# Kernel optimization log

Hardware: AMD Instinct MI355X
Metric: run time of the kernel (lower is better)

Reference implementation:

```python
import jax, jax.numpy as jnp
import numpy as np

EPS = 1e-5  # torch BatchNorm1d default eps

# BinActive: sign forward, straight-through estimator backward (grad clipped where |x|>1)
@jax.custom_vjp
def bin_active(x):
    return jnp.sign(x)

def _ba_fwd(x):
    return jnp.sign(x), x

def _ba_bwd(x, g):
    return (g * (jnp.abs(x) <= 1.0).astype(g.dtype),)

bin_active.defvjp(_ba_fwd, _ba_bwd)

# XNOR-style weight binarization: sign(W) * mean(|W|) per output column, STE backward
@jax.custom_vjp
def bin_weight(w):
    alpha = jnp.mean(jnp.abs(w), axis=0, keepdims=True)  # [1, out]
    return jnp.sign(w) * alpha

def _bw_fwd(w):
    alpha = jnp.mean(jnp.abs(w), axis=0, keepdims=True)
    return jnp.sign(w) * alpha, w

def _bw_bwd(w, g):
    return (g * (jnp.abs(w) <= 1.0).astype(g.dtype),)

bin_weight.defvjp(_bw_fwd, _bw_bwd)


def setup_inputs() -> dict:
    key = jax.random.key(0)
    ks = jax.random.split(key, 8)
    N, E, IN, H, OUT = 100000, 1600000, 256, 128, 40
    x = jax.random.normal(ks[0], (N, IN), dtype=jnp.float32)
    edge_index = jax.random.randint(ks[1], (2, E), 0, N, dtype=jnp.int64)
    W0 = jax.random.normal(ks[2], (IN, H), dtype=jnp.float32) * (2.0 / IN) ** 0.5
    b0 = jnp.zeros((H,), dtype=jnp.float32)
    W1 = jax.random.normal(ks[3], (H, H), dtype=jnp.float32) * (2.0 / H) ** 0.5
    b1 = jnp.zeros((H,), dtype=jnp.float32)
    W2 = jax.random.normal(ks[4], (H, OUT), dtype=jnp.float32) * (2.0 / H) ** 0.5
    b2 = jnp.zeros((OUT,), dtype=jnp.float32)
    return {"x": x, "edge_index": edge_index, "W0": W0, "b0": b0,
            "W1": W1, "b1": b1, "W2": W2, "b2": b2}


def reference(x, edge_index, W0, b0, W1, b1, W2, b2):
    n = x.shape[0]
    loop = jnp.arange(n, dtype=edge_index.dtype)
    src = jnp.concatenate([edge_index[0], loop])  # add self loops (GCN norm)
    dst = jnp.concatenate([edge_index[1], loop])
    deg = jax.ops.segment_sum(jnp.ones_like(src, dtype=x.dtype), dst, num_segments=n)
    dinv = jnp.where(deg > 0, deg ** -0.5, 0.0)
    norm = (dinv[src] * dinv[dst])[:, None]  # [E+N, 1]

    # BatchNorm1d(affine=False), training-mode batch statistics (biased var)
    mu = jnp.mean(x, axis=0)
    var = jnp.var(x, axis=0)
    h = (x - mu) * jax.lax.rsqrt(var + EPS)

    for W, b in ((W0, b0), (W1, b1), (W2, b2)):
        h = bin_active(h)                       # sign binarize (dropout skipped: eval)
        h = h @ bin_weight(W)                   # binary-weight linear
        h = jax.ops.segment_sum(h[src] * norm, dst, num_segments=n) + b  # D^-1/2 (A+I) D^-1/2 agg
    return jax.nn.log_softmax(h, axis=1)
```

## Files before the change

kernel.cpp:

```cpp
#include <hip/hip_runtime.h>
#include <math.h>

#define IN_DIM 256
#define HD 128
#define OUT_DIM 40
#define S2_STRIDE 64
#define NB_CS 1024
#define NXCD 8

__device__ __forceinline__ int xcc_id() {
    int x;
    asm volatile("s_getreg_b32 %0, hwreg(HW_REG_XCC_ID)" : "=s"(x));
    return x & (NXCD - 1);
}

__global__ __launch_bounds__(256) void k_init(unsigned* deg8b, float* muacc8, int NW8) {
    int i = blockIdx.x * 256 + threadIdx.x;
    if (i < NW8) deg8b[i] = 0u;
    if (i < NXCD * 256) muacc8[i] = 0.f;
}

__global__ __launch_bounds__(256) void k_fuse1(const float* __restrict__ x, int N,
                                               float* __restrict__ muacc8,
                                               const int* __restrict__ ei, int E,
                                               unsigned* __restrict__ deg8b, int NW,
                                               int* __restrict__ rank, int ebl,
                                               const float* __restrict__ W0,
                                               const float* __restrict__ W1,
                                               const float* __restrict__ W2,
                                               unsigned long long* W0p,
                                               unsigned long long* W1p,
                                               unsigned long long* W2p,
                                               float* aS0, float* aS1, float* aS2) {
    __shared__ float lds[256];
    int b = blockIdx.x, tid = threadIdx.x;
    if (b < NB_CS) {
        size_t F4 = (size_t)N * (IN_DIM / 4);
        size_t stride = (size_t)NB_CS * 256;
        float a0 = 0.f, a1 = 0.f, a2 = 0.f, a3 = 0.f;
        const float4* x4 = (const float4*)x;
        for (size_t i = (size_t)b * 256 + tid; i < F4; i += stride) {
            float4 v = x4[i];
            a0 += v.x; a1 += v.y; a2 += v.z; a3 += v.w;
        }
        lds[tid] = 0.f;
        __syncthreads();
        int c0 = (tid * 4) & 255;
        atomicAdd(&lds[c0], a0);
        atomicAdd(&lds[c0 + 1], a1);
        atomicAdd(&lds[c0 + 2], a2);
        atomicAdd(&lds[c0 + 3], a3);
        __syncthreads();
        int xc = xcc_id();
        __hip_atomic_fetch_add(&muacc8[xc * 256 + tid], lds[tid],
                               __ATOMIC_RELAXED, __HIP_MEMORY_SCOPE_WORKGROUP);
    } else if (b < NB_CS + ebl) {
        int e = (b - NB_CS) * 256 + tid;
        if (e < E) {
            int d = ei[E + e];
            int xc = xcc_id();
            int sh = 8 * (d & 3);
            unsigned old = __hip_atomic_fetch_add(&deg8b[(size_t)xc * NW + (d >> 2)],
                                                  1u << sh,
                                                  __ATOMIC_RELAXED, __HIP_MEMORY_SCOPE_WORKGROUP);
            rank[e] = (int)((old >> sh) & 0xFFu) | (xc << 28);
        }
    } else {
        int b2 = b - NB_CS - ebl;
        int lane = tid & 63, w = tid >> 6;
        if (b2 < 32) {
            int j = b2 * 4 + w;
            float asum = 0.f;
            unsigned long long words[4];
            #pragma unroll
            for (int q = 0; q < 4; ++q) {
                float v = W0[(size_t)(4 * lane + q) * HD + j];
                asum += fabsf(v);
                words[q] = __ballot(v < 0.f);
            }
            #pragma unroll
            for (int off = 32; off; off >>= 1) asum += __shfl_xor(asum, off);
            if (lane == 0) {
                aS0[j] = 2.f * asum / 256.f;
                #pragma unroll
                for (int q = 0; q < 4; ++q) W0p[j * 4 + q] = words[q];
            }
        } else if (b2 < 64) {
            int j = (b2 - 32) * 4 + w;
            int fl = lane & 15, kk = lane >> 4;
            float asum = 0.f;
            unsigned long long words[2];
            #pragma unroll
            for (int q = 0; q < 2; ++q) {
                float v = W1[(size_t)(fl * 8 + 4 * q + kk) * HD + j];
                asum += fabsf(v);
                words[q] = __ballot(v < 0.f);
            }
            #pragma unroll
            for (int off = 32; off; off >>= 1) asum += __shfl_xor(asum, off);
            if (lane == 0) {
                aS1[j] = 2.f * asum / 128.f;
                W1p[j * 2 + 0] = words[0];
                W1p[j * 2 + 1] = words[1];
            }
        } else {
            int j = (b2 - 64) * 4 + w;
            int fl = lane & 15, kk = lane >> 4;
            if (j < OUT_DIM) {
                float asum = 0.f;
                unsigned long long words[2];
                #pragma unroll
                for (int q = 0; q < 2; ++q) {
                    float v = W2[(size_t)(fl * 8 + 4 * q + kk) * OUT_DIM + j];
                    asum += fabsf(v);
                    words[q] = __ballot(v < 0.f);
                }
                #pragma unroll
                for (int off = 32; off; off >>= 1) asum += __shfl_xor(asum, off);
                if (lane == 0) {
                    aS2[j] = 2.f * asum / 128.f;
                    W2p[j * 2 + 0] = words[0];
                    W2p[j * 2 + 1] = words[1];
                }
            }
        }
    }
}

__global__ __launch_bounds__(256) void k_bp(const unsigned* __restrict__ deg8b, int NW, int N,
                                            int* bp, unsigned long long* __restrict__ xoffp,
                                            float* __restrict__ dinv, int* __restrict__ cnt) {
    __shared__ int sm[256];
    int i = blockIdx.x * 256 + threadIdx.x;
    int c = 0;
    if (i < N) {
        int w = i >> 2, sh = 8 * (i & 3);
        int run = 0;
        unsigned long long pack = 0;
        #pragma unroll
        for (int xc = 0; xc < NXCD; ++xc) {
            unsigned bc = (deg8b[(size_t)xc * NW + w] >> sh) & 0xFFu;
            pack |= (unsigned long long)(unsigned)run << (8 * xc);
            run += (int)bc;
        }
        xoffp[i] = pack;
        c = run;
        cnt[i] = run;
        dinv[i] = (float)(1.0 / sqrt((double)(run + 1)));
    }
    sm[threadIdx.x] = c;
    __syncthreads();
    for (int off = 128; off; off >>= 1) {
        if (threadIdx.x < off) sm[threadIdx.x] += sm[threadIdx.x + off];
        __syncthreads();
    }
    if (threadIdx.x == 0) bp[blockIdx.x] = sm[0];
}

__global__ __launch_bounds__(512) void k_scanbp(const int* __restrict__ bp, int NB, int* bps,
                                                const float* __restrict__ muacc8,
                                                float* __restrict__ mu) {
    __shared__ int sm[512];
    int t = threadIdx.x;
    if (t < 256) {
        float s = 0.f;
        #pragma unroll
        for (int xc = 0; xc < NXCD; ++xc) s += muacc8[xc * 256 + t];
        mu[t] = s;
    }
    int v = (t < NB) ? bp[t] : 0;
    sm[t] = v;
    __syncthreads();
    for (int off = 1; off < 512; off <<= 1) {
        int add = (t >= off) ? sm[t - off] : 0;
        __syncthreads();
        sm[t] += add;
        __syncthreads();
    }
    if (t < NB) bps[t] = sm[t] - v;
}

__global__ __launch_bounds__(256) void k_rowptr(const int* __restrict__ cnt,
                                                const int* __restrict__ bps, int N, int E,
                                                int* row_ptr) {
    __shared__ int wsum[4];
    int t = threadIdx.x, lane = t & 63, w = t >> 6;
    int i = blockIdx.x * 256 + t;
    int c = (i < N) ? cnt[i] : 0;
    int v = c;
    #pragma unroll
    for (int off = 1; off < 64; off <<= 1) {
        int n = __shfl_up(v, off);
        if (lane >= off) v += n;
    }
    if (lane == 63) wsum[w] = v;
    __syncthreads();
    int wo = 0;
    for (int k = 0; k < w; ++k) wo += wsum[k];
    int excl = bps[blockIdx.x] + wo + v - c;
    if (i < N) row_ptr[i] = excl;
    if (blockIdx.x == 0 && t == 0) row_ptr[N] = E;
}

__global__ __launch_bounds__(256) void k_fuse2(const int* __restrict__ ei, int E,
                                               const int* __restrict__ rowp,
                                               const int* __restrict__ rank,
                                               const unsigned long long* __restrict__ xoffp,
                                               int* __restrict__ cs4, int nbScat,
                                               const float* __restrict__ x,
                                               const float* __restrict__ muacc, float inv_n,
                                               const unsigned long long* __restrict__ W0p,
                                               unsigned char* __restrict__ S0, int N) {
    __shared__ unsigned long long w0s[576];
    int b = blockIdx.x, tid = threadIdx.x;
    if (b < nbScat) {
        int e = b * 256 + tid;
        if (e >= E) return;
        int s = ei[e];
        int d = ei[E + e];
        unsigned r = (unsigned)rank[e];
        int xc = (int)(r >> 28);
        int lr = (int)(r & 0xFFu);
        int xo = (int)((xoffp[d] >> (8 * xc)) & 0xFFu);
        int pos = rowp[d] + xo + lr;
        __builtin_nontemporal_store(s, &cs4[pos]);
    } else {
        {
            int i = tid;
            w0s[9 * (i >> 3) + (i & 7)] = W0p[i];
            i = tid + 256;
            w0s[9 * (i >> 3) + (i & 7)] = W0p[i];
        }
        __syncthreads();
        int lane = tid & 63;
        int row = (b - nbScat) * 4 + (tid >> 6);
        if (row >= N) return;
        float4 xv = ((const float4*)(x + (size_t)row * IN_DIM))[lane];
        float4 ms = ((const float4*)muacc)[lane];
        unsigned long long xw[4];
        xw[0] = __ballot(xv.x < ms.x * inv_n);
        xw[1] = __ballot(xv.y < ms.y * inv_n);
        xw[2] = __ballot(xv.z < ms.z * inv_n);
        xw[3] = __ballot(xv.w < ms.w * inv_n);
        unsigned int pack = 0;
        #pragma unroll
        for (int t2 = 0; t2 < 2; ++t2) {
            const unsigned long long* wc = &w0s[9 * lane + 4 * t2];
            int dd = __popcll(xw[0] ^ wc[0]) + __popcll(xw[1] ^ wc[1]) +
                     __popcll(xw[2] ^ wc[2]) + __popcll(xw[3] ^ wc[3]);
            int S = IN_DIM - 2 * dd;
            int s8 = S >> 1;
            if (s8 > 127) s8 = 127;
            pack |= ((unsigned int)(s8 + 128) & 0xffu) << (8 * t2);
        }
        *(unsigned short*)(S0 + (size_t)row * HD + 2 * lane) = (unsigned short)pack;
    }
}

template <int OUTC>
__global__ __launch_bounds__(256) void k_agg_mm(const unsigned char* __restrict__ Sin,
                                                const int* __restrict__ row_ptr,
                                                const int* __restrict__ cs4,
                                                const float* __restrict__ dinv,
                                                const float* __restrict__ alphaS,
                                                const float* __restrict__ bias,
                                                const unsigned long long* __restrict__ Wnp,
                                                unsigned char* __restrict__ Sout, int N) {
    __shared__ unsigned long long wsm[OUTC * 2 + OUTC / 4 + 8];
    int tid = threadIdx.x;
    for (int i = tid; i < OUTC * 2; i += 256) wsm[9 * (i >> 3) + (i & 7)] = Wnp[i];
    __syncthreads();
    int lane = tid & 63;
    int d = blockIdx.x * 4 + (tid >> 6);
    if (d >= N) return;
    int sub = lane >> 4;
    int fl  = lane & 15;
    float dv = dinv[d];
    float acc[8];
    #pragma unroll
    for (int k = 0; k < 8; ++k) acc[k] = 0.f;
    if (sub == 0) {
        float nrm = dv * dv;
        unsigned long long r = *(const unsigned long long*)(Sin + (size_t)d * HD + fl * 8);
        unsigned int lo = (unsigned int)r, hi = (unsigned int)(r >> 32);
        #pragma unroll
        for (int k = 0; k < 4; ++k) {
            acc[k]     = fmaf(nrm, (float)((lo >> (8 * k)) & 0xffu) - 128.f, acc[k]);
            acc[k + 4] = fmaf(nrm, (float)((hi >> (8 * k)) & 0xffu) - 128.f, acc[k + 4]);
        }
    }
    int e0 = row_ptr[d], e1 = row_ptr[d + 1];
    int e = e0 + sub;
    for (; e + 12 < e1; e += 16) {
        int s0_ = cs4[e], s1_ = cs4[e + 4], s2_ = cs4[e + 8], s3_ = cs4[e + 12];
        float n0 = dinv[s0_] * dv, n1 = dinv[s1_] * dv;
        float n2 = dinv[s2_] * dv, n3 = dinv[s3_] * dv;
        unsigned long long r0 = *(const unsigned long long*)(Sin + (size_t)s0_ * HD + fl * 8);
        unsigned long long r1 = *(const unsigned long long*)(Sin + (size_t)s1_ * HD + fl * 8);
        unsigned long long r2 = *(const unsigned long long*)(Sin + (size_t)s2_ * HD + fl * 8);
        unsigned long long r3 = *(const unsigned long long*)(Sin + (size_t)s3_ * HD + fl * 8);
        #pragma unroll
        for (int k = 0; k < 4; ++k) {
            acc[k]     = fmaf(n0, (float)(((unsigned int)r0 >> (8 * k)) & 0xffu) - 128.f, acc[k]);
            acc[k + 4] = fmaf(n0, (float)(((unsigned int)(r0 >> 32) >> (8 * k)) & 0xffu) - 128.f, acc[k + 4]);
            acc[k]     = fmaf(n1, (float)(((unsigned int)r1 >> (8 * k)) & 0xffu) - 128.f, acc[k]);
            acc[k + 4] = fmaf(n1, (float)(((unsigned int)(r1 >> 32) >> (8 * k)) & 0xffu) - 128.f, acc[k + 4]);
            acc[k]     = fmaf(n2, (float)(((unsigned int)r2 >> (8 * k)) & 0xffu) - 128.f, acc[k]);
            acc[k + 4] = fmaf(n2, (float)(((unsigned int)(r2 >> 32) >> (8 * k)) & 0xffu) - 128.f, acc[k + 4]);
            acc[k]     = fmaf(n3, (float)(((unsigned int)r3 >> (8 * k)) & 0xffu) - 128.f, acc[k]);
            acc[k + 4] = fmaf(n3, (float)(((unsigned int)(r3 >> 32) >> (8 * k)) & 0xffu) - 128.f, acc[k + 4]);
        }
    }
    for (; e + 4 < e1; e += 8) {
        int sa = cs4[e], sb = cs4[e + 4];
        float na = dinv[sa] * dv, nb = dinv[sb] * dv;
        unsigned long long ra = *(const unsigned long long*)(Sin + (size_t)sa * HD + fl * 8);
        unsigned long long rb = *(const unsigned long long*)(Sin + (size_t)sb * HD + fl * 8);
        unsigned int la = (unsigned int)ra, ha = (unsigned int)(ra >> 32);
        unsigned int lb = (unsigned int)rb, hb = (unsigned int)(rb >> 32);
        #pragma unroll
        for (int k = 0; k < 4; ++k) {
            acc[k]     = fmaf(na, (float)((la >> (8 * k)) & 0xffu) - 128.f, acc[k]);
            acc[k + 4] = fmaf(na, (float)((ha >> (8 * k)) & 0xffu) - 128.f, acc[k + 4]);
            acc[k]     = fmaf(nb, (float)((lb >> (8 * k)) & 0xffu) - 128.f, acc[k]);
            acc[k + 4] = fmaf(nb, (float)((hb >> (8 * k)) & 0xffu) - 128.f, acc[k + 4]);
        }
    }
    if (e < e1) {
        int s = cs4[e];
        float nrm = dinv[s] * dv;
        unsigned long long r = *(const unsigned long long*)(Sin + (size_t)s * HD + fl * 8);
        unsigned int lo = (unsigned int)r, hi = (unsigned int)(r >> 32);
        #pragma unroll
        for (int k = 0; k < 4; ++k) {
            acc[k]     = fmaf(nrm, (float)((lo >> (8 * k)) & 0xffu) - 128.f, acc[k]);
            acc[k + 4] = fmaf(nrm, (float)((hi >> (8 * k)) & 0xffu) - 128.f, acc[k + 4]);
        }
    }
    #pragma unroll
    for (int k = 0; k < 8; ++k) {
        acc[k] += __shfl_xor(acc[k], 16);
        acc[k] += __shfl_xor(acc[k], 32);
    }
    unsigned int m8 = 0;
    #pragma unroll
    for (int k = 0; k < 8; ++k) {
        int f = fl * 8 + k;
        float v = alphaS[f] * acc[k] + bias[f];
        if (v < 0.f) m8 |= (1u << k);
    }
    unsigned long long x0 = 0, x1 = 0;
    #pragma unroll
    for (int k = 0; k < 4; ++k) {
        unsigned long long bk = __ballot((m8 >> k) & 1u);
        x0 |= (bk & 0xffffULL) << (16 * k);
    }
    #pragma unroll
    for (int k = 4; k < 8; ++k) {
        unsigned long long bk = __ballot((m8 >> k) & 1u);
        x1 |= (bk & 0xffffULL) << (16 * (k - 4));
    }
    if (OUTC == 128) {
        unsigned int pack = 0;
        #pragma unroll
        for (int t2 = 0; t2 < 2; ++t2) {
            int j = 2 * lane + t2;
            int i0 = j * 2;
            const unsigned long long* wc = &wsm[9 * (i0 >> 3) + (i0 & 7)];
            int dd = __popcll(x0 ^ wc[0]) + __popcll(x1 ^ wc[1]);
            int S = HD - 2 * dd;
            pack |= ((unsigned int)((S >> 1) + 128) & 0xffu) << (8 * t2);
        }
        *(unsigned short*)(Sout + (size_t)d * HD + 2 * lane) = (unsigned short)pack;
    } else {
        int p8 = 128;
        if (lane < OUTC) {
            int i0 = lane * 2;
            const unsigned long long* wc = &wsm[9 * (i0 >> 3) + (i0 & 7)];
            int dd = __popcll(x0 ^ wc[0]) + __popcll(x1 ^ wc[1]);
            p8 = ((HD - 2 * dd) >> 1) + 128;
        }
        Sout[(size_t)d * S2_STRIDE + lane] = (unsigned char)p8;
    }
}

__global__ __launch_bounds__(256) void k_agg_out(const unsigned char* __restrict__ S2,
                                                 const int* __restrict__ row_ptr,
                                                 const int* __restrict__ cs4,
                                                 const float* __restrict__ dinv,
                                                 const float* __restrict__ alphaS2,
                                                 const float* __restrict__ b2,
                                                 float* __restrict__ out, int N) {
    int tid = threadIdx.x, lane = tid & 63;
    int d = blockIdx.x * 4 + (tid >> 6);
    if (d >= N) return;
    int sub = lane >> 4;
    int fl  = lane & 15;
    float dv = dinv[d];
    float acc[4] = {0.f, 0.f, 0.f, 0.f};
    if (sub == 0) {
        float nrm = dv * dv;
        unsigned int r4 = *(const unsigned int*)(S2 + (size_t)d * S2_STRIDE + fl * 4);
        #pragma unroll
        for (int k = 0; k < 4; ++k)
            acc[k] = fmaf(nrm, (float)((r4 >> (8 * k)) & 0xffu) - 128.f, acc[k]);
    }
    int e0 = row_ptr[d], e1 = row_ptr[d + 1];
    int e = e0 + sub;
    for (; e + 12 < e1; e += 16) {
        int s0_ = cs4[e], s1_ = cs4[e + 4], s2_ = cs4[e + 8], s3_ = cs4[e + 12];
        float n0 = dinv[s0_] * dv, n1 = dinv[s1_] * dv;
        float n2 = dinv[s2_] * dv, n3 = dinv[s3_] * dv;
        unsigned int r0 = *(const unsigned int*)(S2 + (size_t)s0_ * S2_STRIDE + fl * 4);
        unsigned int r1 = *(const unsigned int*)(S2 + (size_t)s1_ * S2_STRIDE + fl * 4);
        unsigned int r2 = *(const unsigned int*)(S2 + (size_t)s2_ * S2_STRIDE + fl * 4);
        unsigned int r3 = *(const unsigned int*)(S2 + (size_t)s3_ * S2_STRIDE + fl * 4);
        #pragma unroll
        for (int k = 0; k < 4; ++k) {
            acc[k] = fmaf(n0, (float)((r0 >> (8 * k)) & 0xffu) - 128.f, acc[k]);
            acc[k] = fmaf(n1, (float)((r1 >> (8 * k)) & 0xffu) - 128.f, acc[k]);
            acc[k] = fmaf(n2, (float)((r2 >> (8 * k)) & 0xffu) - 128.f, acc[k]);
            acc[k] = fmaf(n3, (float)((r3 >> (8 * k)) & 0xffu) - 128.f, acc[k]);
        }
    }
    for (; e + 4 < e1; e += 8) {
        int sa = cs4[e], sb = cs4[e + 4];
        float na = dinv[sa] * dv, nb = dinv[sb] * dv;
        unsigned int ra = *(const unsigned int*)(S2 + (size_t)sa * S2_STRIDE + fl * 4);
        unsigned int rb = *(const unsigned int*)(S2 + (size_t)sb * S2_STRIDE + fl * 4);
        #pragma unroll
        for (int k = 0; k < 4; ++k) {
            acc[k] = fmaf(na, (float)((ra >> (8 * k)) & 0xffu) - 128.f, acc[k]);
            acc[k] = fmaf(nb, (float)((rb >> (8 * k)) & 0xffu) - 128.f, acc[k]);
        }
    }
    if (e < e1) {
        int s = cs4[e];
        float nrm = dinv[s] * dv;
        unsigned int r4 = *(const unsigned int*)(S2 + (size_t)s * S2_STRIDE + fl * 4);
        #pragma unroll
        for (int k = 0; k < 4; ++k)
            acc[k] = fmaf(nrm, (float)((r4 >> (8 * k)) & 0xffu) - 128.f, acc[k]);
    }
    #pragma unroll
    for (int k = 0; k < 4; ++k) {
        acc[k] += __shfl_xor(acc[k], 16);
        acc[k] += __shfl_xor(acc[k], 32);
    }
    float h[4];
    float mymax = -INFINITY;
    #pragma unroll
    for (int k = 0; k < 4; ++k) {
        int f = fl * 4 + k;
        h[k] = (f < OUT_DIM) ? (alphaS2[f] * acc[k] + b2[f]) : -INFINITY;
        mymax = fmaxf(mymax, h[k]);
    }
    #pragma unroll
    for (int off = 1; off < 16; off <<= 1) mymax = fmaxf(mymax, __shfl_xor(mymax, off));
    float s4 = 0.f;
    #pragma unroll
    for (int k = 0; k < 4; ++k) {
        if (fl * 4 + k < OUT_DIM) s4 += expf(h[k] - mymax);
    }
    #pragma unroll
    for (int off = 1; off < 16; off <<= 1) s4 += __shfl_xor(s4, off);
    float lse = mymax + logf(s4);
    if (sub == 0 && fl < OUT_DIM / 4) {
        float4 o;
        o.x = h[0] - lse; o.y = h[1] - lse; o.z = h[2] - lse; o.w = h[3] - lse;
        *(float4*)(out + (size_t)d * OUT_DIM + fl * 4) = o;
    }
}

extern "C" void kernel_launch(void* const* d_in, const int* in_sizes, int n_in,
                              void* d_out, int out_size, void* d_ws, size_t ws_size,
                              hipStream_t stream) {
    const float* x  = (const float*)d_in[0];
    const int*   ei = (const int*)d_in[1];
    const float* W0 = (const float*)d_in[2];
    const float* b0 = (const float*)d_in[3];
    const float* W1 = (const float*)d_in[4];
    const float* b1 = (const float*)d_in[5];
    const float* W2 = (const float*)d_in[6];
    const float* b2 = (const float*)d_in[7];
    float* out = (float*)d_out;

    int N = in_sizes[0] / IN_DIM;
    int E = in_sizes[1] / 2;
    int NW = (N + 3) / 4;

    char* ws = (char*)d_ws;
    size_t off = 0;
    auto alloc = [&](size_t bytes) -> void* {
        off = (off + 255) & ~(size_t)255;
        void* p = (void*)(ws + off);
        off += bytes;
        return p;
    };
    float* mu     = (float*)alloc(256 * 4);
    float* muacc8 = (float*)alloc(NXCD * 256 * 4);
    unsigned* deg8b = (unsigned*)alloc((size_t)NXCD * NW * 4);
    unsigned long long* xoffp = (unsigned long long*)alloc((size_t)N * 8);
    int*   cnt    = (int*)alloc((size_t)N * 4);
    float* dinv   = (float*)alloc((size_t)N * 4);
    int*   rowp   = (int*)alloc(((size_t)N + 1) * 4);
    int*   bp     = (int*)alloc(512 * 4);
    int*   bps    = (int*)alloc(512 * 4);
    int*   rank   = (int*)alloc((size_t)E * 4);
    int*   cs4    = (int*)alloc((size_t)E * 4);
    unsigned char* S0 = (unsigned char*)alloc((size_t)N * HD);
    unsigned char* S1 = (unsigned char*)alloc((size_t)N * HD);
    unsigned char* S2 = (unsigned char*)alloc((size_t)N * S2_STRIDE);
    unsigned long long* W0p = (unsigned long long*)alloc(128 * 4 * 8);
    unsigned long long* W1p = (unsigned long long*)alloc(128 * 2 * 8);
    unsigned long long* W2p = (unsigned long long*)alloc(40 * 2 * 8);
    float* aS0 = (float*)alloc(128 * 4);
    float* aS1 = (float*)alloc(128 * 4);
    float* aS2 = (float*)alloc(40 * 4);

    int nb256 = (N + 255) / 256;
    int ebl = (E + 255) / 256;
    int NW8 = NXCD * NW;
    int nbInit = (NW8 + 255) / 256;
    float inv_n = 1.0f / (float)N;

    k_init<<<dim3(nbInit), dim3(256), 0, stream>>>(deg8b, muacc8, NW8);
    k_fuse1<<<dim3(NB_CS + ebl + 74), dim3(256), 0, stream>>>(
        x, N, muacc8, ei, E, deg8b, NW, rank, ebl, W0, W1, W2, W0p, W1p, W2p, aS0, aS1, aS2);
    k_bp<<<dim3(nb256), dim3(256), 0, stream>>>(deg8b, NW, N, bp, xoffp, dinv, cnt);
    k_scanbp<<<dim3(1), dim3(512), 0, stream>>>(bp, nb256, bps, muacc8, mu);
    k_rowptr<<<dim3(nb256), dim3(256), 0, stream>>>(cnt, bps, N, E, rowp);

    int nb4 = (N + 3) / 4;
    k_fuse2<<<dim3(ebl + nb4), dim3(256), 0, stream>>>(
        ei, E, rowp, rank, xoffp, cs4, ebl, x, mu, inv_n, W0p, S0, N);
    k_agg_mm<128><<<dim3(nb4), dim3(256), 0, stream>>>(S0, rowp, cs4, dinv, aS0, b0, W1p, S1, N);
    k_agg_mm<40><<<dim3(nb4), dim3(256), 0, stream>>>(S1, rowp, cs4, dinv, aS1, b1, W2p, S2, N);
    k_agg_out<<<dim3(nb4), dim3(256), 0, stream>>>(S2, rowp, cs4, dinv, aS2, b2, out, N);
    (void)out_size; (void)ws_size; (void)n_in;
}
```

Before: 489.0 us.

## Replace global-atomic degree counting with LDS range-partitioned histogram and scatter

The degree count and CSR scatter now use 256 blocks, each owning one of 8 edge chunks and one of 32 node ranges. Each block histograms its destination range in LDS instead of doing global per-XCD byte-packed atomics. The scatter recomputes local ranks with LDS atomics, which removes the per-edge rank array and the large zero-init. The trade-off is that every block scans its whole edge chunk (32x redundant reads of the dst array) and parallelism drops to 256 blocks. The aggregation decode loops are also refactored into a helper.

```diff
diff --git a/kernel.cpp b/kernel.cpp
--- a/kernel.cpp
+++ b/kernel.cpp
@@ -7,6 +7,9 @@
 #define S2_STRIDE 64
 #define NB_CS 1024
 #define NXCD 8
+#define NCHUNK 8
+#define NRANGE 32
+#define RMAX 3200
 
 __device__ __forceinline__ int xcc_id() {
     int x;
@@ -14,17 +17,15 @@
     return x & (NXCD - 1);
 }
 
-__global__ __launch_bounds__(256) void k_init(unsigned* deg8b, float* muacc8, int NW8) {
+__global__ __launch_bounds__(256) void k_init(float* muacc8) {
     int i = blockIdx.x * 256 + threadIdx.x;
-    if (i < NW8) deg8b[i] = 0u;
     if (i < NXCD * 256) muacc8[i] = 0.f;
 }
 
 __global__ __launch_bounds__(256) void k_fuse1(const float* __restrict__ x, int N,
                                                float* __restrict__ muacc8,
                                                const int* __restrict__ ei, int E,
-                                               unsigned* __restrict__ deg8b, int NW,
-                                               int* __restrict__ rank, int ebl,
+                                               unsigned short* __restrict__ cntH,
                                                const float* __restrict__ W0,
                                                const float* __restrict__ W1,
                                                const float* __restrict__ W2,
@@ -32,9 +33,10 @@
                                                unsigned long long* W1p,
                                                unsigned long long* W2p,
                                                float* aS0, float* aS1, float* aS2) {
-    __shared__ float lds[256];
+    __shared__ __align__(16) unsigned ldsbuf[RMAX];
     int b = blockIdx.x, tid = threadIdx.x;
     if (b < NB_CS) {
+        float* lds = (float*)ldsbuf;
         size_t F4 = (size_t)N * (IN_DIM / 4);
         size_t stride = (size_t)NB_CS * 256;
         float a0 = 0.f, a1 = 0.f, a2 = 0.f, a3 = 0.f;
@@ -54,19 +56,43 @@
         int xc = xcc_id();
         __hip_atomic_fetch_add(&muacc8[xc * 256 + tid], lds[tid],
                                __ATOMIC_RELAXED, __HIP_MEMORY_SCOPE_WORKGROUP);
-    } else if (b < NB_CS + ebl) {
-        int e = (b - NB_CS) * 256 + tid;
-        if (e < E) {
-            int d = ei[E + e];
-            int xc = xcc_id();
-            int sh = 8 * (d & 3);
-            unsigned old = __hip_atomic_fetch_add(&deg8b[(size_t)xc * NW + (d >> 2)],
-                                                  1u << sh,
-                                                  __ATOMIC_RELAXED, __HIP_MEMORY_SCOPE_WORKGROUP);
-            rank[e] = (int)((old >> sh) & 0xFFu) | (xc << 28);
-        }
+    } else if (b < NB_CS + NCHUNK * NRANGE) {
+        int bid2 = b - NB_CS;
+        int c = bid2 & (NCHUNK - 1), r = bid2 >> 3;
+        for (int i = tid; i < RMAX; i += 256) ldsbuf[i] = 0u;
+        __syncthreads();
+        int R = (N + NRANGE - 1) / NRANGE;
+        int base = r * R;
+        int lim = N - base; if (lim > R) lim = R; if (lim < 0) lim = 0;
+        int chunk = ((E + NCHUNK - 1) / NCHUNK + 3) & ~3;
+        int eBeg = c * chunk, eEnd = E < eBeg + chunk ? E : eBeg + chunk;
+        const int* dptr = ei + E;
+        int e = eBeg;
+        if ((((unsigned)(E + eBeg)) & 3u) == 0) {
+            int n4 = (eEnd - eBeg) >> 2;
+            const int4* d4 = (const int4*)(dptr + eBeg);
+            for (int i = tid; i < n4; i += 256) {
+                int4 v = d4[i];
+                unsigned r0 = (unsigned)(v.x - base);
+                unsigned r1 = (unsigned)(v.y - base);
+                unsigned r2 = (unsigned)(v.z - base);
+                unsigned r3 = (unsigned)(v.w - base);
+                if (r0 < (unsigned)lim) atomicAdd(&ldsbuf[r0], 1u);
+                if (r1 < (unsigned)lim) atomicAdd(&ldsbuf[r1], 1u);
+                if (r2 < (unsigned)lim) atomicAdd(&ldsbuf[r2], 1u);
+                if (r3 < (unsigned)lim) atomicAdd(&ldsbuf[r3], 1u);
+            }
+            e = eBeg + (n4 << 2);
+        }
+        for (e += tid; e < eEnd; e += 256) {
+            unsigned rel = (unsigned)(dptr[e] - base);
+            if (rel < (unsigned)lim) atomicAdd(&ldsbuf[rel], 1u);
+        }
+        __syncthreads();
+        for (int i = tid; i < lim; i += 256)
+            cntH[(size_t)c * N + base + i] = (unsigned short)ldsbuf[i];
     } else {
-        int b2 = b - NB_CS - ebl;
+        int b2 = b - NB_CS - NCHUNK * NRANGE;
         int lane = tid & 63, w = tid >> 6;
         if (b2 < 32) {
             int j = b2 * 4 + w;
@@ -127,20 +153,19 @@
     }
 }
 
-__global__ __launch_bounds__(256) void k_bp(const unsigned* __restrict__ deg8b, int NW, int N,
+__global__ __launch_bounds__(256) void k_bp(const unsigned short* __restrict__ cntH, int N,
                                             int* bp, unsigned long long* __restrict__ xoffp,
                                             float* __restrict__ dinv, int* __restrict__ cnt) {
     __shared__ int sm[256];
     int i = blockIdx.x * 256 + threadIdx.x;
     int c = 0;
     if (i < N) {
-        int w = i >> 2, sh = 8 * (i & 3);
         int run = 0;
         unsigned long long pack = 0;
         #pragma unroll
-        for (int xc = 0; xc < NXCD; ++xc) {
-            unsigned bc = (deg8b[(size_t)xc * NW + w] >> sh) & 0xFFu;
-            pack |= (unsigned long long)(unsigned)run << (8 * xc);
+        for (int h = 0; h < NCHUNK; ++h) {
+            unsigned bc = cntH[(size_t)h * N + i];
+            pack |= (unsigned long long)(unsigned)run << (8 * h);
             run += (int)bc;
         }
         xoffp[i] = pack;
@@ -204,27 +229,57 @@
 
 __global__ __launch_bounds__(256) void k_fuse2(const int* __restrict__ ei, int E,
                                                const int* __restrict__ rowp,
-                                               const int* __restrict__ rank,
                                                const unsigned long long* __restrict__ xoffp,
-                                               int* __restrict__ cs4, int nbScat,
+                                               int* __restrict__ cs4,
                                                const float* __restrict__ x,
                                                const float* __restrict__ muacc, float inv_n,
                                                const unsigned long long* __restrict__ W0p,
                                                unsigned char* __restrict__ S0, int N) {
-    __shared__ unsigned long long w0s[576];
+    __shared__ __align__(16) unsigned sh32[RMAX];
     int b = blockIdx.x, tid = threadIdx.x;
-    if (b < nbScat) {
-        int e = b * 256 + tid;
-        if (e >= E) return;
-        int s = ei[e];
-        int d = ei[E + e];
-        unsigned r = (unsigned)rank[e];
-        int xc = (int)(r >> 28);
-        int lr = (int)(r & 0xFFu);
-        int xo = (int)((xoffp[d] >> (8 * xc)) & 0xFFu);
-        int pos = rowp[d] + xo + lr;
-        __builtin_nontemporal_store(s, &cs4[pos]);
+    if (b < NCHUNK * NRANGE) {
+        int c = b & (NCHUNK - 1), r = b >> 3;
+        for (int i = tid; i < RMAX; i += 256) sh32[i] = 0u;
+        __syncthreads();
+        int R = (N + NRANGE - 1) / NRANGE;
+        int base = r * R;
+        int lim = N - base; if (lim > R) lim = R; if (lim < 0) lim = 0;
+        int chunk = ((E + NCHUNK - 1) / NCHUNK + 3) & ~3;
+        int eBeg = c * chunk, eEnd = E < eBeg + chunk ? E : eBeg + chunk;
+        int e = eBeg;
+        if (((unsigned)eBeg & 3u) == 0 && (((unsigned)(E + eBeg)) & 3u) == 0) {
+            int n4 = (eEnd - eBeg) >> 2;
+            const int4* s4p = (const int4*)(ei + eBeg);
+            const int4* d4p = (const int4*)(ei + E + eBeg);
+            for (int i = tid; i < n4; i += 256) {
+                int4 sv = s4p[i];
+                int4 dv = d4p[i];
+                int ss[4] = {sv.x, sv.y, sv.z, sv.w};
+                int dd[4] = {dv.x, dv.y, dv.z, dv.w};
+                #pragma unroll
+                for (int k = 0; k < 4; ++k) {
+                    unsigned rel = (unsigned)(dd[k] - base);
+                    if (rel < (unsigned)lim) {
+                        unsigned lr = atomicAdd(&sh32[rel], 1u);
+                        int pos = rowp[dd[k]] +
+                                  (int)((xoffp[dd[k]] >> (8 * c)) & 0xFFu) + (int)lr;
+                        cs4[pos] = ss[k];
+                    }
+                }
+            }
+            e = eBeg + (n4 << 2);
+        }
+        for (e += tid; e < eEnd; e += 256) {
+            int d = ei[E + e];
+            unsigned rel = (unsigned)(d - base);
+            if (rel < (unsigned)lim) {
+                unsigned lr = atomicAdd(&sh32[rel], 1u);
+                int pos = rowp[d] + (int)((xoffp[d] >> (8 * c)) & 0xFFu) + (int)lr;
+                cs4[pos] = ei[e];
+            }
+        }
     } else {
+        unsigned long long* w0s = (unsigned long long*)sh32;
         {
             int i = tid;
             w0s[9 * (i >> 3) + (i & 7)] = W0p[i];
@@ -233,7 +288,7 @@
         }
         __syncthreads();
         int lane = tid & 63;
-        int row = (b - nbScat) * 4 + (tid >> 6);
+        int row = (b - NCHUNK * NRANGE) * 4 + (tid >> 6);
         if (row >= N) return;
         float4 xv = ((const float4*)(x + (size_t)row * IN_DIM))[lane];
         float4 ms = ((const float4*)muacc)[lane];
@@ -255,6 +310,13 @@
         }
         *(unsigned short*)(S0 + (size_t)row * HD + 2 * lane) = (unsigned short)pack;
     }
+}
+
+__device__ __forceinline__ void acc4s(float n, unsigned v, float* a) {
+    a[0] = fmaf(n, (float)(v & 0xffu) - 128.f, a[0]);
+    a[1] = fmaf(n, (float)((v >> 8) & 0xffu) - 128.f, a[1]);
+    a[2] = fmaf(n, (float)((v >> 16) & 0xffu) - 128.f, a[2]);
+    a[3] = fmaf(n, (float)(v >> 24) - 128.f, a[3]);
 }
 
 template <int OUTC>
@@ -281,13 +343,9 @@
     for (int k = 0; k < 8; ++k) acc[k] = 0.f;
     if (sub == 0) {
         float nrm = dv * dv;
-        unsigned long long r = *(const unsigned long long*)(Sin + (size_t)d * HD + fl * 8);
-        unsigned int lo = (unsigned int)r, hi = (unsigned int)(r >> 32);
-        #pragma unroll
-        for (int k = 0; k < 4; ++k) {
-            acc[k]     = fmaf(nrm, (float)((lo >> (8 * k)) & 0xffu) - 128.f, acc[k]);
-            acc[k + 4] = fmaf(nrm, (float)((hi >> (8 * k)) & 0xffu) - 128.f, acc[k + 4]);
-        }
+        unsigned long long rr = *(const unsigned long long*)(Sin + (size_t)d * HD + fl * 8);
+        acc4s(nrm, (unsigned)rr, acc);
+        acc4s(nrm, (unsigned)(rr >> 32), acc + 4);
     }
     int e0 = row_ptr[d], e1 = row_ptr[d + 1];
     int e = e0 + sub;
@@ -299,43 +357,25 @@
         unsigned long long r1 = *(const unsigned long long*)(Sin + (size_t)s1_ * HD + fl * 8);
         unsigned long long r2 = *(const unsigned long long*)(Sin + (size_t)s2_ * HD + fl * 8);
         unsigned long long r3 = *(const unsigned long long*)(Sin + (size_t)s3_ * HD + fl * 8);
-        #pragma unroll
-        for (int k = 0; k < 4; ++k) {
-            acc[k]     = fmaf(n0, (float)(((unsigned int)r0 >> (8 * k)) & 0xffu) - 128.f, acc[k]);
-            acc[k + 4] = fmaf(n0, (float)(((unsigned int)(r0 >> 32) >> (8 * k)) & 0xffu) - 128.f, acc[k + 4]);
-            acc[k]     = fmaf(n1, (float)(((unsigned int)r1 >> (8 * k)) & 0xffu) - 128.f, acc[k]);
-            acc[k + 4] = fmaf(n1, (float)(((unsigned int)(r1 >> 32) >> (8 * k)) & 0xffu) - 128.f, acc[k + 4]);
-            acc[k]     = fmaf(n2, (float)(((unsigned int)r2 >> (8 * k)) & 0xffu) - 128.f, acc[k]);
-            acc[k + 4] = fmaf(n2, (float)(((unsigned int)(r2 >> 32) >> (8 * k)) & 0xffu) - 128.f, acc[k + 4]);
-            acc[k]     = fmaf(n3, (float)(((unsigned int)r3 >> (8 * k)) & 0xffu) - 128.f, acc[k]);
-            acc[k + 4] = fmaf(n3, (float)(((unsigned int)(r3 >> 32) >> (8 * k)) & 0xffu) - 128.f, acc[k + 4]);
-        }
+        acc4s(n0, (unsigned)r0, acc); acc4s(n0, (unsigned)(r0 >> 32), acc + 4);
+        acc4s(n1, (unsigned)r1, acc); acc4s(n1, (unsigned)(r1 >> 32), acc + 4);
+        acc4s(n2, (unsigned)r2, acc); acc4s(n2, (unsigned)(r2 >> 32), acc + 4);
+        acc4s(n3, (unsigned)r3, acc); acc4s(n3, (unsigned)(r3 >> 32), acc + 4);
     }
     for (; e + 4 < e1; e += 8) {
         int sa = cs4[e], sb = cs4[e + 4];
         float na = dinv[sa] * dv, nb = dinv[sb] * dv;
         unsigned long long ra = *(const unsigned long long*)(Sin + (size_t)sa * HD + fl * 8);
         unsigned long long rb = *(const unsigned long long*)(Sin + (size_t)sb * HD + fl * 8);
-        unsigned int la = (unsigned int)ra, ha = (unsigned int)(ra >> 32);
-        unsigned int lb = (unsigned int)rb, hb = (unsigned int)(rb >> 32);
-        #pragma unroll
-        for (int k = 0; k < 4; ++k) {
-            acc[k]     = fmaf(na, (float)((la >> (8 * k)) & 0xffu) - 128.f, acc[k]);
-            acc[k + 4] = fmaf(na, (float)((ha >> (8 * k)) & 0xffu) - 128.f, acc[k + 4]);
-            acc[k]     = fmaf(nb, (float)((lb >> (8 * k)) & 0xffu) - 128.f, acc[k]);
-            acc[k + 4] = fmaf(nb, (float)((hb >> (8 * k)) & 0xffu) - 128.f, acc[k + 4]);
-        }
+        acc4s(na, (unsigned)ra, acc); acc4s(na, (unsigned)(ra >> 32), acc + 4);
+        acc4s(nb, (unsigned)rb, acc); acc4s(nb, (unsigned)(rb >> 32), acc + 4);
     }
     if (e < e1) {
         int s = cs4[e];
         float nrm = dinv[s] * dv;
-        unsigned long long r = *(const unsigned long long*)(Sin + (size_t)s * HD + fl * 8);
-        unsigned int lo = (unsigned int)r, hi = (unsigned int)(r >> 32);
-        #pragma unroll
-        for (int k = 0; k < 4; ++k) {
-            acc[k]     = fmaf(nrm, (float)((lo >> (8 * k)) & 0xffu) - 128.f, acc[k]);
-            acc[k + 4] = fmaf(nrm, (float)((hi >> (8 * k)) & 0xffu) - 128.f, acc[k + 4]);
-        }
+        unsigned long long rr = *(const unsigned long long*)(Sin + (size_t)s * HD + fl * 8);
+        acc4s(nrm, (unsigned)rr, acc);
+        acc4s(nrm, (unsigned)(rr >> 32), acc + 4);
     }
     #pragma unroll
     for (int k = 0; k < 8; ++k) {
@@ -401,9 +441,7 @@
     if (sub == 0) {
         float nrm = dv * dv;
         unsigned int r4 = *(const unsigned int*)(S2 + (size_t)d * S2_STRIDE + fl * 4);
-        #pragma unroll
-        for (int k = 0; k < 4; ++k)
-            acc[k] = fmaf(nrm, (float)((r4 >> (8 * k)) & 0xffu) - 128.f, acc[k]);
+        acc4s(nrm, r4, acc);
     }
     int e0 = row_ptr[d], e1 = row_ptr[d + 1];
     int e = e0 + sub;
@@ -415,32 +453,24 @@
         unsigned int r1 = *(const unsigned int*)(S2 + (size_t)s1_ * S2_STRIDE + fl * 4);
         unsigned int r2 = *(const unsigned int*)(S2 + (size_t)s2_ * S2_STRIDE + fl * 4);
         unsigned int r3 = *(const unsigned int*)(S2 + (size_t)s3_ * S2_STRIDE + fl * 4);
-        #pragma unroll
-        for (int k = 0; k < 4; ++k) {
-            acc[k] = fmaf(n0, (float)((r0 >> (8 * k)) & 0xffu) - 128.f, acc[k]);
-            acc[k] = fmaf(n1, (float)((r1 >> (8 * k)) & 0xffu) - 128.f, acc[k]);
-            acc[k] = fmaf(n2, (float)((r2 >> (8 * k)) & 0xffu) - 128.f, acc[k]);
-            acc[k] = fmaf(n3, (float)((r3 >> (8 * k)) & 0xffu) - 128.f, acc[k]);
-        }
+        acc4s(n0, r0, acc);
+        acc4s(n1, r1, acc);
+        acc4s(n2, r2, acc);
+        acc4s(n3, r3, acc);
     }
     for (; e + 4 < e1; e += 8) {
         int sa = cs4[e], sb = cs4[e + 4];
         float na = dinv[sa] * dv, nb = dinv[sb] * dv;
         unsigned int ra = *(const unsigned int*)(S2 + (size_t)sa * S2_STRIDE + fl * 4);
         unsigned int rb = *(const unsigned int*)(S2 + (size_t)sb * S2_STRIDE + fl * 4);
-        #pragma unroll
-        for (int k = 0; k < 4; ++k) {
-            acc[k] = fmaf(na, (float)((ra >> (8 * k)) & 0xffu) - 128.f, acc[k]);
-            acc[k] = fmaf(nb, (float)((rb >> (8 * k)) & 0xffu) - 128.f, acc[k]);
-        }
+        acc4s(na, ra, acc);
+        acc4s(nb, rb, acc);
     }
     if (e < e1) {
         int s = cs4[e];
         float nrm = dinv[s] * dv;
         unsigned int r4 = *(const unsigned int*)(S2 + (size_t)s * S2_STRIDE + fl * 4);
-        #pragma unroll
-        for (int k = 0; k < 4; ++k)
-            acc[k] = fmaf(nrm, (float)((r4 >> (8 * k)) & 0xffu) - 128.f, acc[k]);
+        acc4s(nrm, r4, acc);
     }
     #pragma unroll
     for (int k = 0; k < 4; ++k) {
@@ -487,7 +517,6 @@
 
     int N = in_sizes[0] / IN_DIM;
     int E = in_sizes[1] / 2;
-    int NW = (N + 3) / 4;
 
     char* ws = (char*)d_ws;
     size_t off = 0;
@@ -499,14 +528,13 @@
     };
     float* mu     = (float*)alloc(256 * 4);
     float* muacc8 = (float*)alloc(NXCD * 256 * 4);
-    unsigned* deg8b = (unsigned*)alloc((size_t)NXCD * NW * 4);
+    unsigned short* cntH = (unsigned short*)alloc((size_t)NCHUNK * N * 2);
     unsigned long long* xoffp = (unsigned long long*)alloc((size_t)N * 8);
     int*   cnt    = (int*)alloc((size_t)N * 4);
     float* dinv   = (float*)alloc((size_t)N * 4);
     int*   rowp   = (int*)alloc(((size_t)N + 1) * 4);
     int*   bp     = (int*)alloc(512 * 4);
     int*   bps    = (int*)alloc(512 * 4);
-    int*   rank   = (int*)alloc((size_t)E * 4);
     int*   cs4    = (int*)alloc((size_t)E * 4);
     unsigned char* S0 = (unsigned char*)alloc((size_t)N * HD);
     unsigned char* S1 = (unsigned char*)alloc((size_t)N * HD);
@@ -519,21 +547,18 @@
     float* aS2 = (float*)alloc(40 * 4);
 
     int nb256 = (N + 255) / 256;
-    int ebl = (E + 255) / 256;
-    int NW8 = NXCD * NW;
-    int nbInit = (NW8 + 255) / 256;
     float inv_n = 1.0f / (float)N;
 
-    k_init<<<dim3(nbInit), dim3(256), 0, stream>>>(deg8b, muacc8, NW8);
-    k_fuse1<<<dim3(NB_CS + ebl + 74), dim3(256), 0, stream>>>(
-        x, N, muacc8, ei, E, deg8b, NW, rank, ebl, W0, W1, W2, W0p, W1p, W2p, aS0, aS1, aS2);
-    k_bp<<<dim3(nb256), dim3(256), 0, stream>>>(deg8b, NW, N, bp, xoffp, dinv, cnt);
+    k_init<<<dim3(8), dim3(256), 0, stream>>>(muacc8);
+    k_fuse1<<<dim3(NB_CS + NCHUNK * NRANGE + 74), dim3(256), 0, stream>>>(
+        x, N, muacc8, ei, E, cntH, W0, W1, W2, W0p, W1p, W2p, aS0, aS1, aS2);
+    k_bp<<<dim3(nb256), dim3(256), 0, stream>>>(cntH, N, bp, xoffp, dinv, cnt);
     k_scanbp<<<dim3(1), dim3(512), 0, stream>>>(bp, nb256, bps, muacc8, mu);
     k_rowptr<<<dim3(nb256), dim3(256), 0, stream>>>(cnt, bps, N, E, rowp);
 
     int nb4 = (N + 3) / 4;
-    k_fuse2<<<dim3(ebl + nb4), dim3(256), 0, stream>>>(
-        ei, E, rowp, rank, xoffp, cs4, ebl, x, mu, inv_n, W0p, S0, N);
+    k_fuse2<<<dim3(NCHUNK * NRANGE + nb4), dim3(256), 0, stream>>>(
+        ei, E, rowp, xoffp, cs4, x, mu, inv_n, W0p, S0, N);
     k_agg_mm<128><<<dim3(nb4), dim3(256), 0, stream>>>(S0, rowp, cs4, dinv, aS0, b0, W1p, S1, N);
     k_agg_mm<40><<<dim3(nb4), dim3(256), 0, stream>>>(S1, rowp, cs4, dinv, aS1, b1, W2p, S2, N);
     k_agg_out<<<dim3(nb4), dim3(256), 0, stream>>>(S2, rowp, cs4, dinv, aS2, b2, out, N);
```

After: 686.4 us. 1.4x slower.
